# Kernel tuning notes

Hardware: AMD Instinct MI355X
Metric: run time of the kernel (lower is better)

Reference implementation:

```python
import jax, jax.numpy as jnp
import numpy as np

N_STREAMS = 8
D = 2048
N_HEADS = 16
HEAD_DIM = D // N_HEADS
STREAM_DIM = D // N_STREAMS
EPS = 1e-6


def rmsnorm(x, w):
    return x * jax.lax.rsqrt(jnp.mean(x * x, axis=-1, keepdims=True) + EPS) * w


def sinkhorn_knopp(phi, iterations=15):
    M = jnp.exp(phi)
    for _ in range(iterations):
        M = M / jnp.sum(M, axis=1, keepdims=True)
        M = M / jnp.sum(M, axis=0, keepdims=True)
    return M


def setup_inputs() -> dict:
    key = jax.random.key(0)
    ks = jax.random.split(key, 16)
    B, T = 2, 2048
    s = 0.02
    return {
        "x": jax.random.normal(ks[0], (B, T, D), jnp.float32),
        "rope_cos": jax.random.uniform(ks[1], (T, HEAD_DIM), jnp.float32),
        "rope_sin": jax.random.uniform(ks[2], (T, HEAD_DIM), jnp.float32),
        "gate_w": jax.random.normal(ks[3], (3 * N_STREAMS, D), jnp.float32) * s,
        "gate_b": jnp.zeros((3 * N_STREAMS,), jnp.float32),
        "phi_res": jax.random.normal(ks[4], (N_STREAMS, N_STREAMS), jnp.float32) * s,
        "ln1_w": jnp.ones((D,), jnp.float32),
        "ln2_w": jnp.ones((D,), jnp.float32),
        "in_proj_w": jax.random.normal(ks[5], (3 * D, D), jnp.float32) * s,
        "in_proj_b": jnp.zeros((3 * D,), jnp.float32),
        "out_proj_w": jax.random.normal(ks[6], (D, D), jnp.float32) * s,
        "out_proj_b": jnp.zeros((D,), jnp.float32),
        "mlp_w1": jax.random.normal(ks[7], (4 * D, D), jnp.float32) * s,
        "mlp_b1": jnp.zeros((4 * D,), jnp.float32),
        "mlp_w2": jax.random.normal(ks[8], (D, 4 * D), jnp.float32) * s,
        "mlp_b2": jnp.zeros((D,), jnp.float32),
    }


def reference(x, rope_cos, rope_sin, gate_w, gate_b, phi_res, ln1_w, ln2_w,
              in_proj_w, in_proj_b, out_proj_w, out_proj_b,
              mlp_w1, mlp_b1, mlp_w2, mlp_b2):
    B, T, _ = x.shape
    n = N_STREAMS

    # ---- Sinkhorn-gated multi-stream residual mixing ----
    x_state = jnp.mean(x, axis=1)                              # [B, D]
    gates = x_state @ gate_w.T + gate_b                        # [B, 3n]
    g_res = jax.nn.sigmoid(gates[:, 2 * n:])                   # [B, n]
    H_res = sinkhorn_knopp(phi_res, 15)                        # [n, n]
    x_streams = x.reshape(B, T, n, STREAM_DIM)
    # out[b,t,m,d] = sum_n H[m,n] * g[b,n] * x_streams[b,t,n,d]
    mhc_out = jnp.einsum('mn,bn,btnd->btmd', H_res, g_res, x_streams).reshape(B, T, D)

    # ---- causal multi-head attention ----
    normed = rmsnorm(x, ln1_w)
    qkv = normed @ in_proj_w.T + in_proj_b                     # [B, T, 3D]
    q, k, v = jnp.split(qkv, 3, axis=-1)
    def heads(t):
        return t.reshape(B, T, N_HEADS, HEAD_DIM).transpose(0, 2, 1, 3)
    q, k, v = heads(q), heads(k), heads(v)                     # [B, H, T, hd]
    scores = jnp.einsum('bhqd,bhkd->bhqk', q, k) / jnp.sqrt(jnp.float32(HEAD_DIM))
    causal = jnp.tril(jnp.ones((T, T), bool))
    scores = jnp.where(causal, scores, jnp.finfo(scores.dtype).min)
    probs = jax.nn.softmax(scores, axis=-1)
    attn = jnp.einsum('bhqk,bhkd->bhqd', probs, v)
    attn = attn.transpose(0, 2, 1, 3).reshape(B, T, D)
    attn_out = attn @ out_proj_w.T + out_proj_b

    x2 = x + attn_out

    # ---- MLP (exact GELU, dropout is identity in eval) ----
    normed2 = rmsnorm(x2, ln2_w)
    h = jax.nn.gelu(normed2 @ mlp_w1.T + mlp_b1, approximate=False)
    ffn_out = h @ mlp_w2.T + mlp_b2

    return x2 + ffn_out + mhc_out
```

## Files before the change

### kernel.cpp

```cpp
#include <hip/hip_runtime.h>
#include <hip/hip_bf16.h>

#define DD 2048
#define TT 2048
#define NHEAD 16
#define HDIM 128
#define QKVN 6144

typedef __attribute__((ext_vector_type(8))) short short8;
typedef __attribute__((ext_vector_type(4))) float f32x4;

__device__ __forceinline__ short f2bf(float f) {
  __hip_bfloat16 h = __float2bfloat16(f);
  return *reinterpret_cast<short*>(&h);
}

__device__ __forceinline__ f32x4 mfma_bf16(short8 a, short8 b, f32x4 c) {
  return __builtin_amdgcn_mfma_f32_16x16x32_bf16(a, b, c, 0, 0, 0);
}

__device__ __forceinline__ float gelu_exact(float v) {
  return 0.5f * v * (1.0f + erff(v * 0.70710678118654752440f));
}

__global__ __launch_bounds__(256) void cvt_bf16_kernel(const float* __restrict__ in,
                                                       short* __restrict__ outp) {
  const size_t i = ((size_t)blockIdx.x * 256 + threadIdx.x) * 8;
  const f32x4 a = *(const f32x4*)&in[i];
  const f32x4 b = *(const f32x4*)&in[i + 4];
  short8 o;
#pragma unroll
  for (int e = 0; e < 4; ++e) { o[e] = f2bf(a[e]); o[e + 4] = f2bf(b[e]); }
  *(short8*)&outp[i] = o;
}

__global__ __launch_bounds__(256) void mean_partial_kernel(const float* __restrict__ x,
                                                           float* __restrict__ part) {
  const int d = blockIdx.x * 256 + threadIdx.x;
  const int y = blockIdx.y;
  const int b = y >> 3, tc = y & 7;
  const float* p = x + (size_t)b * TT * DD + (size_t)tc * 256 * DD + d;
  float s = 0.f;
#pragma unroll 4
  for (int t = 0; t < 256; ++t) s += p[(size_t)t * DD];
  part[(size_t)y * DD + d] = s;
}

__global__ __launch_bounds__(256) void gates_kernel(const float* __restrict__ part,
                                                    const float* __restrict__ gw,
                                                    const float* __restrict__ gb,
                                                    float* __restrict__ g) {
  const int bm = blockIdx.x;
  const int b = bm >> 3, mm = bm & 7;
  const int j = 16 + mm;
  float acc = 0.f;
  for (int d = threadIdx.x; d < DD; d += 256) {
    float xv = 0.f;
#pragma unroll
    for (int tc = 0; tc < 8; ++tc) xv += part[(size_t)(b * 8 + tc) * DD + d];
    acc += xv * (1.f / TT) * gw[(size_t)j * DD + d];
  }
#pragma unroll
  for (int d = 1; d < 64; d <<= 1) acc += __shfl_xor(acc, d);
  __shared__ float ws4[4];
  if ((threadIdx.x & 63) == 0) ws4[threadIdx.x >> 6] = acc;
  __syncthreads();
  if (threadIdx.x == 0) {
    const float tot = ws4[0] + ws4[1] + ws4[2] + ws4[3] + gb[j];
    g[bm] = 1.f / (1.f + __expf(-tot));
  }
}

__global__ void sinkhorn_kernel(const float* __restrict__ phi, float* __restrict__ H) {
  __shared__ float M[64];
  const int t = threadIdx.x;
  const int i = t >> 3, j = t & 7;
  M[t] = __expf(phi[t]);
  __syncthreads();
  for (int it = 0; it < 15; ++it) {
    float rs = 0.f;
#pragma unroll
    for (int jj = 0; jj < 8; ++jj) rs += M[i * 8 + jj];
    float v = M[t] / rs;
    __syncthreads(); M[t] = v; __syncthreads();
    float cs = 0.f;
#pragma unroll
    for (int ii = 0; ii < 8; ++ii) cs += M[ii * 8 + j];
    v = M[t] / cs;
    __syncthreads(); M[t] = v; __syncthreads();
  }
  H[t] = M[t];
}

__global__ __launch_bounds__(256) void rmsnorm_kernel(const float* __restrict__ x,
                                                      const float* __restrict__ wt,
                                                      short* __restrict__ outp) {
  const int row = blockIdx.x;
  const int tid = threadIdx.x;
  const float* xr = x + (size_t)row * DD;
  const f32x4 v0 = *(const f32x4*)&xr[tid * 8];
  const f32x4 v1 = *(const f32x4*)&xr[tid * 8 + 4];
  float ss = 0.f;
#pragma unroll
  for (int e = 0; e < 4; ++e) ss += v0[e] * v0[e] + v1[e] * v1[e];
#pragma unroll
  for (int d = 1; d < 64; d <<= 1) ss += __shfl_xor(ss, d);
  __shared__ float wsum[4];
  if ((tid & 63) == 0) wsum[tid >> 6] = ss;
  __syncthreads();
  const float rstd = rsqrtf((wsum[0] + wsum[1] + wsum[2] + wsum[3]) * (1.f / DD) + 1e-6f);
  const f32x4 w0 = *(const f32x4*)&wt[tid * 8];
  const f32x4 w1 = *(const f32x4*)&wt[tid * 8 + 4];
  short8 ov;
#pragma unroll
  for (int e = 0; e < 4; ++e) {
    ov[e] = f2bf(v0[e] * rstd * w0[e]);
    ov[e + 4] = f2bf(v1[e] * rstd * w1[e]);
  }
  *(short8*)&outp[(size_t)row * DD + tid * 8] = ov;
}

template <int EPI>
__global__ __launch_bounds__(256) void gemm_nt(const short* __restrict__ A,
                                               const short* __restrict__ B,
                                               const float* __restrict__ bias,
                                               void* __restrict__ Cptr,
                                               const float* __restrict__ resid,
                                               int M, int N, int K) {
  __shared__ __align__(16) short As[128 * 64];
  __shared__ __align__(16) short Bs[128 * 64];
  const int tid = threadIdx.x;
  const int lane = tid & 63;
  const int wid = tid >> 6;
  const int bm = blockIdx.x * 128;
  const int bn = blockIdx.y * 128;
  const int wr = (wid >> 1) * 64;
  const int wc = (wid & 1) * 64;
  f32x4 acc[4][4] = {};

  for (int kb = 0; kb < K; kb += 64) {
    __syncthreads();
#pragma unroll
    for (int p = 0; p < 4; ++p) {
      const int flat = p * 2048 + tid * 8;
      const int row = flat >> 6;
      const int col = flat & 63;
      const int dst = (row << 6) | (((col >> 3) ^ (row & 7)) << 3);
      *(int4*)&As[dst] = *(const int4*)&A[(size_t)(bm + row) * K + kb + col];
      *(int4*)&Bs[dst] = *(const int4*)&B[(size_t)(bn + row) * K + kb + col];
    }
    __syncthreads();
#pragma unroll
    for (int kk = 0; kk < 64; kk += 32) {
      short8 af[4], bfr[4];
#pragma unroll
      for (int i = 0; i < 4; ++i) {
        const int row = wr + i * 16 + (lane & 15);
        const int ch = ((kk >> 3) + (lane >> 4)) ^ (row & 7);
        af[i] = *(const short8*)&As[(row << 6) | (ch << 3)];
      }
#pragma unroll
      for (int j = 0; j < 4; ++j) {
        const int row = wc + j * 16 + (lane & 15);
        const int ch = ((kk >> 3) + (lane >> 4)) ^ (row & 7);
        bfr[j] = *(const short8*)&Bs[(row << 6) | (ch << 3)];
      }
#pragma unroll
      for (int i = 0; i < 4; ++i)
#pragma unroll
        for (int j = 0; j < 4; ++j)
          acc[i][j] = mfma_bf16(af[i], bfr[j], acc[i][j]);
    }
  }

  const int r0 = bm + wr + (lane >> 4) * 4;
  const int c0 = bn + wc + (lane & 15);
#pragma unroll
  for (int i = 0; i < 4; ++i) {
#pragma unroll
    for (int j = 0; j < 4; ++j) {
      const int col = c0 + j * 16;
      const float bv = bias[col];
#pragma unroll
      for (int r = 0; r < 4; ++r) {
        const int row = r0 + i * 16 + r;
        const float v = acc[i][j][r] + bv;
        if constexpr (EPI == 0) {
          ((float*)Cptr)[(size_t)row * N + col] = v;
        } else if constexpr (EPI == 1) {
          ((short*)Cptr)[(size_t)row * N + col] = f2bf(gelu_exact(v));
        } else if constexpr (EPI == 2) {
          ((float*)Cptr)[(size_t)row * N + col] = v + resid[(size_t)row * N + col];
        } else {
          ((short*)Cptr)[(size_t)row * N + col] = f2bf(v);
        }
      }
    }
  }
}

__global__ __launch_bounds__(256) void flash_attn_kernel(const short* __restrict__ qkv,
                                                         short* __restrict__ attn) {
  const int tid = threadIdx.x;
  const int lane = tid & 63;
  const int w = tid >> 6;
  const int qb = blockIdx.x * 64;
  const int h = blockIdx.y;
  const int b = blockIdx.z;

  __shared__ __align__(16) short Ks[32 * 128];
  __shared__ __align__(16) short Vt[128 * 40];
  __shared__ __align__(16) short Ps[4][512];

  const size_t base = (size_t)b * TT * QKVN;
  const int lr = lane & 15;
  const int lg = lane >> 4;

  const int qrow = qb + w * 16 + lr;
  short8 qf[4];
#pragma unroll
  for (int c = 0; c < 4; ++c)
    qf[c] = *(const short8*)&qkv[base + (size_t)qrow * QKVN + h * HDIM + c * 32 + lg * 8];

  f32x4 o[8] = {};
  float mrow[4] = {-1e30f, -1e30f, -1e30f, -1e30f};
  float lrow[4] = {0.f, 0.f, 0.f, 0.f};

  const int ntiles = (qb >> 5) + 2;
  for (int t = 0; t < ntiles; ++t) {
    const int kv0 = t * 32;
    __syncthreads();
#pragma unroll
    for (int p = 0; p < 2; ++p) {
      const int flat = p * 2048 + tid * 8;
      const int r = flat >> 7;
      const int c = flat & 127;
      const int dst = (r << 7) | (((c >> 3) ^ (r & 7)) << 3);
      *(int4*)&Ks[dst] = *(const int4*)&qkv[base + (size_t)(kv0 + r) * QKVN + 2048 + h * HDIM + c];
      const short8 vv = *(const short8*)&qkv[base + (size_t)(kv0 + r) * QKVN + 4096 + h * HDIM + c];
#pragma unroll
      for (int e = 0; e < 8; ++e) Vt[(c + e) * 40 + r] = vv[e];
    }
    __syncthreads();

    f32x4 s0 = {}, s1 = {};
#pragma unroll
    for (int c = 0; c < 4; ++c) {
      const int ch = c * 4 + lg;
      const short8 b0 = *(const short8*)&Ks[(lr << 7) | ((ch ^ (lr & 7)) << 3)];
      const short8 b1 = *(const short8*)&Ks[((lr + 16) << 7) | ((ch ^ (lr & 7)) << 3)];
      s0 = mfma_bf16(qf[c], b0, s0);
      s1 = mfma_bf16(qf[c], b1, s1);
    }

    const float sc = 0.08838834764831845f;
    const int qr0 = qb + w * 16 + lg * 4;
    const int cc = kv0 + lr;
    float sv0[4], sv1[4], pm[4];
#pragma unroll
    for (int r = 0; r < 4; ++r) {
      sv0[r] = (cc <= qr0 + r) ? s0[r] * sc : -1e30f;
      sv1[r] = (cc + 16 <= qr0 + r) ? s1[r] * sc : -1e30f;
      pm[r] = fmaxf(sv0[r], sv1[r]);
    }
#pragma unroll
    for (int d = 1; d < 16; d <<= 1) {
#pragma unroll
      for (int r = 0; r < 4; ++r) pm[r] = fmaxf(pm[r], __shfl_xor(pm[r], d));
    }
    float p0[4], p1[4], rs[4];
#pragma unroll
    for (int r = 0; r < 4; ++r) {
      const float mn = fmaxf(mrow[r], pm[r]);
      const float al = __expf(mrow[r] - mn);
      mrow[r] = mn;
      p0[r] = __expf(sv0[r] - mn);
      p1[r] = __expf(sv1[r] - mn);
      rs[r] = p0[r] + p1[r];
      lrow[r] *= al;
#pragma unroll
      for (int ch = 0; ch < 8; ++ch) o[ch][r] *= al;
    }
#pragma unroll
    for (int d = 1; d < 16; d <<= 1) {
#pragma unroll
      for (int r = 0; r < 4; ++r) rs[r] += __shfl_xor(rs[r], d);
    }
#pragma unroll
    for (int r = 0; r < 4; ++r) lrow[r] += rs[r];

#pragma unroll
    for (int r = 0; r < 4; ++r) {
      const int rowp = lg * 4 + r;
      Ps[w][((lr >> 3) << 7) | (rowp << 3) | (lr & 7)] = f2bf(p0[r]);
      Ps[w][(((lr + 16) >> 3) << 7) | (rowp << 3) | (lr & 7)] = f2bf(p1[r]);
    }
    const short8 pf = *(const short8*)&Ps[w][(lg << 7) | (lr << 3)];
#pragma unroll
    for (int ch = 0; ch < 8; ++ch) {
      const short8 vf = *(const short8*)&Vt[(ch * 16 + lr) * 40 + lg * 8];
      o[ch] = mfma_bf16(pf, vf, o[ch]);
    }
  }

#pragma unroll
  for (int ch = 0; ch < 8; ++ch) {
#pragma unroll
    for (int r = 0; r < 4; ++r) {
      const int row = qb + w * 16 + lg * 4 + r;
      const int col = h * HDIM + ch * 16 + lr;
      attn[((size_t)b * TT + row) * DD + col] = f2bf(o[ch][r] / lrow[r]);
    }
  }
}

__global__ __launch_bounds__(256) void final_kernel(const float* __restrict__ x,
                                                    const float* __restrict__ x2,
                                                    const float* __restrict__ ffn,
                                                    const float* __restrict__ H,
                                                    const float* __restrict__ g,
                                                    float* __restrict__ out) {
  const int row = blockIdx.x;
  const int tid = threadIdx.x;
  const int b = row >> 11;
  __shared__ float xs[DD];
  __shared__ float Wmn[64];
  const float* xr = x + (size_t)row * DD;
  *(f32x4*)&xs[tid * 8] = *(const f32x4*)&xr[tid * 8];
  *(f32x4*)&xs[tid * 8 + 4] = *(const f32x4*)&xr[tid * 8 + 4];
  if (tid < 64) Wmn[tid] = H[tid] * g[b * 8 + (tid & 7)];
  __syncthreads();
  const int mm = tid >> 5;
  const int dd0 = (tid * 8) & 255;
  const f32x4 a0 = *(const f32x4*)&x2[(size_t)row * DD + tid * 8];
  const f32x4 a1 = *(const f32x4*)&x2[(size_t)row * DD + tid * 8 + 4];
  const f32x4 f0 = *(const f32x4*)&ffn[(size_t)row * DD + tid * 8];
  const f32x4 f1 = *(const f32x4*)&ffn[(size_t)row * DD + tid * 8 + 4];
  f32x4 o0, o1;
#pragma unroll
  for (int e = 0; e < 8; ++e) {
    float acc = 0.f;
#pragma unroll
    for (int n = 0; n < 8; ++n) acc += Wmn[mm * 8 + n] * xs[n * 256 + dd0 + e];
    if (e < 4) o0[e] = a0[e] + f0[e] + acc;
    else       o1[e - 4] = a1[e - 4] + f1[e - 4] + acc;
  }
  *(f32x4*)&out[(size_t)row * DD + tid * 8] = o0;
  *(f32x4*)&out[(size_t)row * DD + tid * 8 + 4] = o1;
}

extern "C" void kernel_launch(void* const* d_in, const int* in_sizes, int n_in,
                              void* d_out, int out_size, void* d_ws, size_t ws_size,
                              hipStream_t stream) {
  const float* x      = (const float*)d_in[0];
  const float* gate_w = (const float*)d_in[3];
  const float* gate_b = (const float*)d_in[4];
  const float* phi    = (const float*)d_in[5];
  const float* ln1    = (const float*)d_in[6];
  const float* ln2    = (const float*)d_in[7];
  const float* inw    = (const float*)d_in[8];
  const float* inb    = (const float*)d_in[9];
  const float* outw   = (const float*)d_in[10];
  const float* outb   = (const float*)d_in[11];
  const float* w1     = (const float*)d_in[12];
  const float* b1     = (const float*)d_in[13];
  const float* w2     = (const float*)d_in[14];
  const float* b2     = (const float*)d_in[15];
  float* outp = (float*)d_out;
  char* ws = (char*)d_ws;

  short* Wbf  = (short*)(ws + 0);
  short* norm = (short*)(ws + 33554432ull);
  short* qkv  = (short*)(ws + 50331648ull);
  short* attn = (short*)(ws + 100663296ull);
  float* x2   = (float*)(ws + 117440512ull);
  float* ffn  = (float*)(ws + 150994944ull);
  float* part = (float*)(ws + 184549376ull);
  float* g    = (float*)(ws + 184680448ull);
  float* H    = (float*)(ws + 184680512ull);
  short* hbuf = qkv;

  mean_partial_kernel<<<dim3(8, 16), 256, 0, stream>>>(x, part);
  gates_kernel<<<16, 256, 0, stream>>>(part, gate_w, gate_b, g);
  sinkhorn_kernel<<<1, 64, 0, stream>>>(phi, H);

  rmsnorm_kernel<<<4096, 256, 0, stream>>>(x, ln1, norm);
  cvt_bf16_kernel<<<6144, 256, 0, stream>>>(inw, Wbf);
  gemm_nt<3><<<dim3(32, 48), 256, 0, stream>>>(norm, Wbf, inb, qkv, nullptr, 4096, 6144, 2048);
  flash_attn_kernel<<<dim3(32, 16, 2), 256, 0, stream>>>(qkv, attn);
  cvt_bf16_kernel<<<2048, 256, 0, stream>>>(outw, Wbf);
  gemm_nt<2><<<dim3(32, 16), 256, 0, stream>>>(attn, Wbf, outb, x2, x, 4096, 2048, 2048);

  rmsnorm_kernel<<<4096, 256, 0, stream>>>(x2, ln2, norm);
  cvt_bf16_kernel<<<8192, 256, 0, stream>>>(w1, Wbf);
  gemm_nt<1><<<dim3(32, 64), 256, 0, stream>>>(norm, Wbf, b1, hbuf, nullptr, 4096, 8192, 2048);
  cvt_bf16_kernel<<<8192, 256, 0, stream>>>(w2, Wbf);
  gemm_nt<0><<<dim3(32, 16), 256, 0, stream>>>(hbuf, Wbf, b2, ffn, nullptr, 4096, 2048, 8192);

  final_kernel<<<4096, 256, 0, stream>>>(x, x2, ffn, H, g, outp);
}
```

Baseline: 1.260 ms.

## Use direct global-to-LDS loads in GEMM and restructure flash attention pipeline

The GEMM now fills shared memory with global_load_lds instead of loading through registers. The flash attention kernel is rewritten around 64-wide KV tiles. It computes S transposed so P stays in registers without an LDS round trip, and it reads V with ds_read_b64_tr_b16 transpose loads instead of scalar transposed stores. The next KV tile is prefetched into registers while the current one is computed, and fully masked sub-blocks on the diagonal tile are skipped. These changes aim to remove LDS staging overhead, barriers and scalar stores, at the cost of more complex inline asm and register pressure.

```diff
diff --git a/kernel.cpp b/kernel.cpp
--- a/kernel.cpp
+++ b/kernel.cpp
@@ -8,6 +8,7 @@
 #define QKVN 6144
 
 typedef __attribute__((ext_vector_type(8))) short short8;
+typedef __attribute__((ext_vector_type(4))) short s16x4;
 typedef __attribute__((ext_vector_type(4))) float f32x4;
 
 __device__ __forceinline__ short f2bf(float f) {
@@ -22,6 +23,9 @@
 __device__ __forceinline__ float gelu_exact(float v) {
   return 0.5f * v * (1.0f + erff(v * 0.70710678118654752440f));
 }
+
+#define AS1(p) ((const __attribute__((address_space(1))) void*)(p))
+#define AS3(p) ((__attribute__((address_space(3))) void*)(p))
 
 __global__ __launch_bounds__(256) void cvt_bf16_kernel(const float* __restrict__ in,
                                                        short* __restrict__ outp) {
@@ -138,16 +142,18 @@
   const int wc = (wid & 1) * 64;
   f32x4 acc[4][4] = {};
 
+  const int srow_ = tid >> 3;
+  const int scs = (tid & 7) ^ (srow_ & 7);
+
   for (int kb = 0; kb < K; kb += 64) {
     __syncthreads();
 #pragma unroll
     for (int p = 0; p < 4; ++p) {
-      const int flat = p * 2048 + tid * 8;
-      const int row = flat >> 6;
-      const int col = flat & 63;
-      const int dst = (row << 6) | (((col >> 3) ^ (row & 7)) << 3);
-      *(int4*)&As[dst] = *(const int4*)&A[(size_t)(bm + row) * K + kb + col];
-      *(int4*)&Bs[dst] = *(const int4*)&B[(size_t)(bn + row) * K + kb + col];
+      const int row = p * 32 + srow_;
+      const short* gA = &A[(size_t)(bm + row) * K + kb + (scs << 3)];
+      const short* gB = &B[(size_t)(bn + row) * K + kb + (scs << 3)];
+      __builtin_amdgcn_global_load_lds(AS1(gA), AS3(&As[p * 2048 + (tid & 192) * 8]), 16, 0, 0);
+      __builtin_amdgcn_global_load_lds(AS1(gB), AS3(&Bs[p * 2048 + (tid & 192) * 8]), 16, 0, 0);
     }
     __syncthreads();
 #pragma unroll
@@ -204,114 +210,171 @@
   const int tid = threadIdx.x;
   const int lane = tid & 63;
   const int w = tid >> 6;
-  const int qb = blockIdx.x * 64;
+  const int bx = blockIdx.x;
+  const int qb = bx * 64;
   const int h = blockIdx.y;
   const int b = blockIdx.z;
-
-  __shared__ __align__(16) short Ks[32 * 128];
-  __shared__ __align__(16) short Vt[128 * 40];
-  __shared__ __align__(16) short Ps[4][512];
-
-  const size_t base = (size_t)b * TT * QKVN;
   const int lr = lane & 15;
   const int lg = lane >> 4;
 
+  __shared__ __align__(16) short Ks[64 * 128];
+  __shared__ __align__(16) short Vs[64 * 128];
+
+  const size_t base = (size_t)b * (size_t)TT * QKVN;
+
   const int qrow = qb + w * 16 + lr;
   short8 qf[4];
 #pragma unroll
-  for (int c = 0; c < 4; ++c)
-    qf[c] = *(const short8*)&qkv[base + (size_t)qrow * QKVN + h * HDIM + c * 32 + lg * 8];
+  for (int kc = 0; kc < 4; ++kc)
+    qf[kc] = *(const short8*)&qkv[base + (size_t)qrow * QKVN + h * HDIM + kc * 32 + lg * 8];
+
+  const int skv0 = tid >> 4;
+  const int sc_ = tid & 15;
 
   f32x4 o[8] = {};
-  float mrow[4] = {-1e30f, -1e30f, -1e30f, -1e30f};
-  float lrow[4] = {0.f, 0.f, 0.f, 0.f};
-
-  const int ntiles = (qb >> 5) + 2;
+  float m_run = -3e30f, Lpart = 0.f;
+  const int ntiles = bx + 1;
+
+  {
+    int4 rK[4], rV[4];
+#pragma unroll
+    for (int p = 0; p < 4; ++p) {
+      const size_t grow = base + (size_t)(p * 16 + skv0) * QKVN + h * HDIM + sc_ * 8;
+      rK[p] = *(const int4*)&qkv[grow + 2048];
+      rV[p] = *(const int4*)&qkv[grow + 4096];
+    }
+#pragma unroll
+    for (int p = 0; p < 4; ++p) {
+      const int kv = p * 16 + skv0;
+      *(int4*)&Ks[kv * 128 + ((sc_ ^ (skv0 & 7)) << 3)] = rK[p];
+      *(int4*)&Vs[((kv >> 2) * 8 + (sc_ >> 1)) * 64 + (skv0 & 3) * 16 + (sc_ & 1) * 8] = rV[p];
+    }
+  }
+  __syncthreads();
+
+  const unsigned vsoff = (unsigned)(uintptr_t)((__attribute__((address_space(3))) short*)Vs);
+  const unsigned vbl = vsoff + (unsigned)(lg * 1024 + lr * 8);
+
   for (int t = 0; t < ntiles; ++t) {
-    const int kv0 = t * 32;
-    __syncthreads();
-#pragma unroll
-    for (int p = 0; p < 2; ++p) {
-      const int flat = p * 2048 + tid * 8;
-      const int r = flat >> 7;
-      const int c = flat & 127;
-      const int dst = (r << 7) | (((c >> 3) ^ (r & 7)) << 3);
-      *(int4*)&Ks[dst] = *(const int4*)&qkv[base + (size_t)(kv0 + r) * QKVN + 2048 + h * HDIM + c];
-      const short8 vv = *(const short8*)&qkv[base + (size_t)(kv0 + r) * QKVN + 4096 + h * HDIM + c];
-#pragma unroll
-      for (int e = 0; e < 8; ++e) Vt[(c + e) * 40 + r] = vv[e];
-    }
-    __syncthreads();
-
-    f32x4 s0 = {}, s1 = {};
-#pragma unroll
-    for (int c = 0; c < 4; ++c) {
-      const int ch = c * 4 + lg;
-      const short8 b0 = *(const short8*)&Ks[(lr << 7) | ((ch ^ (lr & 7)) << 3)];
-      const short8 b1 = *(const short8*)&Ks[((lr + 16) << 7) | ((ch ^ (lr & 7)) << 3)];
-      s0 = mfma_bf16(qf[c], b0, s0);
-      s1 = mfma_bf16(qf[c], b1, s1);
-    }
-
-    const float sc = 0.08838834764831845f;
-    const int qr0 = qb + w * 16 + lg * 4;
-    const int cc = kv0 + lr;
-    float sv0[4], sv1[4], pm[4];
-#pragma unroll
-    for (int r = 0; r < 4; ++r) {
-      sv0[r] = (cc <= qr0 + r) ? s0[r] * sc : -1e30f;
-      sv1[r] = (cc + 16 <= qr0 + r) ? s1[r] * sc : -1e30f;
-      pm[r] = fmaxf(sv0[r], sv1[r]);
-    }
-#pragma unroll
-    for (int d = 1; d < 16; d <<= 1) {
-#pragma unroll
-      for (int r = 0; r < 4; ++r) pm[r] = fmaxf(pm[r], __shfl_xor(pm[r], d));
-    }
-    float p0[4], p1[4], rs[4];
-#pragma unroll
-    for (int r = 0; r < 4; ++r) {
-      const float mn = fmaxf(mrow[r], pm[r]);
-      const float al = __expf(mrow[r] - mn);
-      mrow[r] = mn;
-      p0[r] = __expf(sv0[r] - mn);
-      p1[r] = __expf(sv1[r] - mn);
-      rs[r] = p0[r] + p1[r];
-      lrow[r] *= al;
-#pragma unroll
-      for (int ch = 0; ch < 8; ++ch) o[ch][r] *= al;
-    }
-#pragma unroll
-    for (int d = 1; d < 16; d <<= 1) {
-#pragma unroll
-      for (int r = 0; r < 4; ++r) rs[r] += __shfl_xor(rs[r], d);
-    }
-#pragma unroll
-    for (int r = 0; r < 4; ++r) lrow[r] += rs[r];
-
-#pragma unroll
-    for (int r = 0; r < 4; ++r) {
-      const int rowp = lg * 4 + r;
-      Ps[w][((lr >> 3) << 7) | (rowp << 3) | (lr & 7)] = f2bf(p0[r]);
-      Ps[w][(((lr + 16) >> 3) << 7) | (rowp << 3) | (lr & 7)] = f2bf(p1[r]);
-    }
-    const short8 pf = *(const short8*)&Ps[w][(lg << 7) | (lr << 3)];
-#pragma unroll
-    for (int ch = 0; ch < 8; ++ch) {
-      const short8 vf = *(const short8*)&Vt[(ch * 16 + lr) * 40 + lg * 8];
-      o[ch] = mfma_bf16(pf, vf, o[ch]);
-    }
-  }
-
-#pragma unroll
-  for (int ch = 0; ch < 8; ++ch) {
+    const bool masked = (t == ntiles - 1);
+    int4 rK[4], rV[4];
+    if (t + 1 < ntiles) {
+      const int kv0n = (t + 1) * 64;
+#pragma unroll
+      for (int p = 0; p < 4; ++p) {
+        const size_t grow = base + (size_t)(kv0n + p * 16 + skv0) * QKVN + h * HDIM + sc_ * 8;
+        rK[p] = *(const int4*)&qkv[grow + 2048];
+        rV[p] = *(const int4*)&qkv[grow + 4096];
+      }
+    }
+
+    f32x4 s[4] = {};
+#pragma unroll
+    for (int kb = 0; kb < 4; ++kb) {
+      if (masked && kb > w) continue;
+#pragma unroll
+      for (int kc = 0; kc < 4; ++kc) {
+        const int row = kb * 16 + lr;
+        const short8 kf = *(const short8*)&Ks[(row << 7) + ((((kc << 2) + lg) ^ (lr & 7)) << 3)];
+        s[kb] = mfma_bf16(kf, qf[kc], s[kb]);
+      }
+    }
+
+    const float scl = 0.08838834764831845f;
+    float sv[4][4];
+    float pm = -3e30f;
+#pragma unroll
+    for (int kb = 0; kb < 4; ++kb)
+#pragma unroll
+      for (int r = 0; r < 4; ++r) {
+        float v = s[kb][r] * scl;
+        if (masked && (kb * 16 + lg * 4 + r > w * 16 + lr)) v = -3e30f;
+        sv[kb][r] = v;
+        pm = fmaxf(pm, v);
+      }
+    pm = fmaxf(pm, __shfl_xor(pm, 16));
+    pm = fmaxf(pm, __shfl_xor(pm, 32));
+    const float mn = fmaxf(m_run, pm);
+    const float al = __expf(m_run - mn);
+    m_run = mn;
+    float ps = 0.f;
+    short pb[16];
+#pragma unroll
+    for (int kb = 0; kb < 4; ++kb)
+#pragma unroll
+      for (int r = 0; r < 4; ++r) {
+        const float p = __expf(sv[kb][r] - mn);
+        ps += p;
+        pb[kb * 4 + r] = f2bf(p);
+      }
+    Lpart = Lpart * al + ps;
+    float alr[4];
+#pragma unroll
+    for (int r = 0; r < 4; ++r) alr[r] = __shfl(al, ((lane >> 4) << 2) + r);
+#pragma unroll
+    for (int ch = 0; ch < 8; ++ch)
+#pragma unroll
+      for (int r = 0; r < 4; ++r) o[ch][r] *= alr[r];
+
+    short8 pa[2];
+#pragma unroll
+    for (int k2 = 0; k2 < 2; ++k2)
+#pragma unroll
+      for (int j = 0; j < 8; ++j) pa[k2][j] = pb[k2 * 8 + j];
+
+#pragma unroll
+    for (int chp = 0; chp < 8; chp += 2) {
+      s16x4 tv[8];
+#pragma unroll
+      for (int c2 = 0; c2 < 2; ++c2)
+#pragma unroll
+        for (int k2 = 0; k2 < 2; ++k2) {
+          const unsigned a0 = vbl + (unsigned)(k2 * 8192 + (chp + c2) * 128);
+          const int ix = c2 * 4 + k2 * 2;
+          asm volatile("ds_read_b64_tr_b16 %0, %2\n\t"
+                       "ds_read_b64_tr_b16 %1, %2 offset:4096"
+                       : "=&v"(tv[ix]), "=&v"(tv[ix + 1])
+                       : "v"(a0));
+        }
+      asm volatile("s_waitcnt lgkmcnt(0)" ::: "memory");
+      __builtin_amdgcn_sched_barrier(0);
+#pragma unroll
+      for (int c2 = 0; c2 < 2; ++c2)
+#pragma unroll
+        for (int k2 = 0; k2 < 2; ++k2) {
+          const int ix = c2 * 4 + k2 * 2;
+          short8 vf;
+#pragma unroll
+          for (int e = 0; e < 4; ++e) { vf[e] = tv[ix][e]; vf[e + 4] = tv[ix + 1][e]; }
+          o[chp + c2] = mfma_bf16(pa[k2], vf, o[chp + c2]);
+        }
+    }
+
+    if (t + 1 < ntiles) {
+      __syncthreads();
+#pragma unroll
+      for (int p = 0; p < 4; ++p) {
+        const int kv = p * 16 + skv0;
+        *(int4*)&Ks[kv * 128 + ((sc_ ^ (skv0 & 7)) << 3)] = rK[p];
+        *(int4*)&Vs[((kv >> 2) * 8 + (sc_ >> 1)) * 64 + (skv0 & 3) * 16 + (sc_ & 1) * 8] = rV[p];
+      }
+      __syncthreads();
+    }
+  }
+
+  float Lq = Lpart;
+  Lq += __shfl_xor(Lq, 16);
+  Lq += __shfl_xor(Lq, 32);
+  float inv[4];
+#pragma unroll
+  for (int r = 0; r < 4; ++r) inv[r] = 1.f / __shfl(Lq, ((lane >> 4) << 2) + r);
+#pragma unroll
+  for (int ch = 0; ch < 8; ++ch)
 #pragma unroll
     for (int r = 0; r < 4; ++r) {
       const int row = qb + w * 16 + lg * 4 + r;
-      const int col = h * HDIM + ch * 16 + lr;
-      attn[((size_t)b * TT + row) * DD + col] = f2bf(o[ch][r] / lrow[r]);
-    }
-  }
+      attn[((size_t)b * TT + row) * DD + h * HDIM + ch * 16 + lr] = f2bf(o[ch][r] * inv[r]);
+    }
 }
 
 __global__ __launch_bounds__(256) void final_kernel(const float* __restrict__ x,
```

New measurement: 1.116 ms. 1.13x faster.
